# Performance work log

Measured on AMD Instinct MI355X. Metric: run time of the kernel, lower is better.

The kernel has to match this reference:

```python
import jax, jax.numpy as jnp
import numpy as np

MG = (5, 5)          # mesh_grid_size
UP = (17, 17)        # upsample_size
IMG = (512.0, 512.0) # image_size
B = 8192
FC_OUT = MG[0] * MG[1] * 2  # 50
KH = (UP[0] - 1) // (MG[0] - 1) + 1  # 5
KW = (UP[1] - 1) // (MG[1] - 1) + 1  # 5
SH = (UP[0] - 1) // (MG[0] - 1)      # 4
SW = (UP[1] - 1) // (MG[1] - 1)      # 4
L0 = MG[0] - 1
L1 = MG[1] - 1


def _grid(h, w):
    # channel 0: x coords vary along rows (image_size[0]); channel 1: y along cols
    x_t = jnp.broadcast_to(jnp.linspace(0.0, IMG[0], h)[:, None], (h, w))
    y_t = jnp.broadcast_to(jnp.linspace(0.0, IMG[1], w)[None, :], (h, w))
    return jnp.stack([x_t, y_t], 0)  # [2, h, w]


def _unfold22(a):
    # a: [B, 2, H, W] -> [B, (H-1)*(W-1), 4, 2]; 4 = kernel positions row-major, 2 = channel
    p = jnp.stack([a[:, :, :-1, :-1], a[:, :, :-1, 1:],
                   a[:, :, 1:, :-1], a[:, :, 1:, 1:]], axis=2)  # [B,2,4,H-1,W-1]
    return p.reshape(a.shape[0], 2, 4, -1).transpose(0, 3, 2, 1)


def _persp(src, dst):
    # exact 4-point homography solve (torchgeometry.get_perspective_transform)
    x0, y0 = src[..., 0], src[..., 1]
    u, v = dst[..., 0], dst[..., 1]
    z = jnp.zeros_like(x0)
    o = jnp.ones_like(x0)
    ax = jnp.stack([x0, y0, o, z, z, z, -u * x0, -u * y0], -1)  # [N,4,8]
    ay = jnp.stack([z, z, z, x0, y0, o, -v * x0, -v * y0], -1)
    A = jnp.concatenate([ax, ay], 1)                 # [N,8,8]
    bb = jnp.concatenate([u, v], 1)[..., None]       # [N,8,1]
    h = jnp.linalg.solve(A, bb)[..., 0]              # [N,8]
    return jnp.concatenate([h, o[:, :1]], 1).reshape(-1, 3, 3)


def setup_inputs() -> dict:
    key = jax.random.key(0)
    ks = jax.random.split(key, 4)
    def lin(k, i, o):
        return jax.random.normal(k, (i, o), jnp.float32) / jnp.sqrt(i)
    return {
        "x": jax.random.normal(ks[0], (B, 1024), jnp.float32),
        "W1": lin(ks[1], 1024, 1024), "b1": jnp.zeros((1024,), jnp.float32),
        "W2": lin(ks[2], 1024, 2048), "b2": jnp.zeros((2048,), jnp.float32),
        "W3": lin(ks[3], 2048, FC_OUT), "b3": jnp.zeros((FC_OUT,), jnp.float32),
    }


def reference(x, W1, b1, W2, b2, W3, b3):
    Bn = x.shape[0]
    h = jax.nn.relu(x @ W1 + b1)
    h = jax.nn.relu(h @ W2 + b2)
    out = (h @ W3 + b3).reshape(Bn, 2, MG[0], MG[1])  # [B,2,5,5] mesh flow

    # sparse control grid and 2x2 patch corner points
    gs = _grid(MG[0], MG[1])
    src = _unfold22(jnp.broadcast_to(gs[None], (Bn, 2, MG[0], MG[1]))).reshape(-1, 4, 2)
    flow = _unfold22(out).reshape(-1, 4, 2)
    M = _persp(src, src + flow)  # [B*16, 3, 3]

    # dense grid and its unfold2 (kernel KHxKW, stride SHxSW) patch points
    gd = _grid(UP[0], UP[1])  # [2, 17, 17]
    gi = (np.arange(L0) * SH)[:, None, None, None] + np.arange(KH)[None, None, :, None]
    gj = (np.arange(L1) * SW)[None, :, None, None] + np.arange(KW)[None, None, None, :]
    I, J = np.broadcast_arrays(gi, gj)  # [L0,L1,KH,KW]
    pts = gd[:, I, J].transpose(1, 2, 3, 4, 0).reshape(1, L0 * L1, KH * KW, 2)
    pts = jnp.broadcast_to(pts, (Bn, L0 * L1, KH * KW, 2)).reshape(Bn * L0 * L1, KH * KW, 2)

    # transform_points: homogeneous warp + perspective divide
    ph = jnp.concatenate([pts, jnp.ones(pts.shape[:-1] + (1,), pts.dtype)], -1)
    oh = jnp.einsum('nij,npj->npi', M, ph)
    warped = oh[..., :2] / oh[..., 2:3]
    warped = warped.reshape(Bn, L0, L1, KH, KW, 2)

    # Fold: scatter-accumulate overlapping patches
    fold = jnp.zeros((Bn, 2, UP[0], UP[1]), x.dtype)
    for i in range(L0):
        for j in range(L1):
            blk = warped[:, i, j].transpose(0, 3, 1, 2)  # [B,2,KH,KW]
            fold = fold.at[:, :, i * SH:i * SH + KH, j * SW:j * SW + KW].add(blk)

    # boundary rescaling exactly as the torch code: only the 5x5 crossing points
    idx = np.arange(0, UP[0], MG[0] - 1)
    X, Y = np.meshgrid(idx, idx, indexing='xy')
    fold = fold.at[:, :, X, Y].multiply(0.5)
    for (a, b) in ((0, 0), (0, UP[1] - 1), (UP[0] - 1, UP[1] - 1), (UP[0] - 1, 0)):
        fold = fold.at[:, :, a, b].multiply(2.0)

    return fold - gd[None]  # upsampled mesh flow [B,2,17,17]
```

## Files before the change

### kernel.cpp

```cpp
#include <hip/hip_runtime.h>

typedef __bf16 bf16x8 __attribute__((ext_vector_type(8)));
typedef float f32x4 __attribute__((ext_vector_type(4)));

__device__ __forceinline__ unsigned short f2bf(float f) {
  unsigned int u = __builtin_bit_cast(unsigned int, f);
  unsigned int r = (u + 0x7fffu + ((u >> 16) & 1u)) >> 16;
  return (unsigned short)r;
}

__device__ __forceinline__ float bf2f(unsigned short u) {
  unsigned int v = ((unsigned int)u) << 16;
  return __builtin_bit_cast(float, v);
}

__device__ __forceinline__ void load16_lds(const unsigned short* g, unsigned short* l) {
  __builtin_amdgcn_global_load_lds(
      (const __attribute__((address_space(1))) void*)g,
      (__attribute__((address_space(3))) void*)l, 16, 0, 0);
}

__device__ __forceinline__ void wait_vm0() {
  asm volatile("s_waitcnt vmcnt(0)" ::: "memory");
  __builtin_amdgcn_sched_barrier(0);
}
__device__ __forceinline__ void wait_lgkm0() {
  asm volatile("s_waitcnt lgkmcnt(0)" ::: "memory");
  __builtin_amdgcn_sched_barrier(0);
}
__device__ __forceinline__ void barrier_raw() {
  __builtin_amdgcn_sched_barrier(0);
  __builtin_amdgcn_s_barrier();
  __builtin_amdgcn_sched_barrier(0);
}


__global__ __launch_bounds__(256) void prepass(
    const float* __restrict__ x, const float* __restrict__ W1,
    const float* __restrict__ W2, const float* __restrict__ W3,
    unsigned short* __restrict__ xbf, unsigned short* __restrict__ w1t,
    unsigned short* __restrict__ w2t, unsigned short* __restrict__ w3t) {
  __shared__ float tile[32][33];
  const int bid = blockIdx.x;
  const int t = threadIdx.x;
  if (bid < 2048) {
    for (int i = bid * 256 + t; i < 2097152; i += 2048 * 256) {
      float4 f = ((const float4*)x)[i];
      uint2 o;
      o.x = (unsigned)f2bf(f.x) | ((unsigned)f2bf(f.y) << 16);
      o.y = (unsigned)f2bf(f.z) | ((unsigned)f2bf(f.w) << 16);
      ((uint2*)xbf)[i] = o;
    }
  } else if (bid < 3072) {
    int ti = bid - 2048;
    int n0 = (ti & 31) * 32, k0 = (ti >> 5) * 32;
    int tx = t & 31, ty = t >> 5;
    #pragma unroll
    for (int r = 0; r < 32; r += 8)
      tile[ty + r][tx] = W1[(size_t)(k0 + ty + r) * 1024 + n0 + tx];
    __syncthreads();
    #pragma unroll
    for (int r = 0; r < 32; r += 8)
      w1t[(size_t)(n0 + ty + r) * 1024 + k0 + tx] = f2bf(tile[tx][ty + r]);
  } else if (bid < 5120) {
    int ti = bid - 3072;
    int n0 = (ti & 63) * 32, k0 = (ti >> 6) * 32;
    int tx = t & 31, ty = t >> 5;
    #pragma unroll
    for (int r = 0; r < 32; r += 8)
      tile[ty + r][tx] = W2[(size_t)(k0 + ty + r) * 2048 + n0 + tx];
    __syncthreads();
    #pragma unroll
    for (int r = 0; r < 32; r += 8)
      w2t[(size_t)(n0 + ty + r) * 1024 + k0 + tx] = f2bf(tile[tx][ty + r]);
  } else {
    int idx = (bid - 5120) * 256 + t;
    int n = idx >> 11, k = idx & 2047;
    w3t[idx] = f2bf((n < 50) ? W3[(size_t)k * 50 + n] : 0.f);
  }
}


__global__ __launch_bounds__(512, 2) void gemm1_8p(
    const unsigned short* __restrict__ A,
    const unsigned short* __restrict__ Bt,
    const float* __restrict__ bias,
    unsigned short* __restrict__ C) {
  constexpr int K = 1024, N = 1024, NT = 16;
  constexpr int AEL = 256 * 64;
  constexpr int BEL = 128 * 64;
  constexpr int BUF = AEL + BEL;
  __shared__ __align__(16) unsigned short smem[2 * BUF];
  const int t = threadIdx.x;
  const int m0 = blockIdx.x * 256;
  const int n0 = blockIdx.y * 128;
  const int lane = t & 63, wv = t >> 6;
  const int l16 = lane & 15, quad = lane >> 4;
  const int wr = wv >> 1, wc = wv & 1;
  const int rb = wr * 64, cb = wc * 64;

  const int srow = t >> 3;
  const int sg = ((t & 7) ^ (srow & 7)) * 8;
  const unsigned short* Ag0 = A + (size_t)(m0 + srow) * K + sg;
  const unsigned short* Bg0 = Bt + (size_t)(n0 + srow) * K + sg;
  const int ldsO = wv * 8 * 64;

  f32x4 acc[4][4] = {};

  #pragma unroll
  for (int r = 0; r < 4; ++r)
    load16_lds(Ag0 + (size_t)(r * 64) * K, &smem[r * 4096 + ldsO]);
  #pragma unroll
  for (int r = 0; r < 2; ++r)
    load16_lds(Bg0 + (size_t)(r * 64) * K, &smem[AEL + r * 4096 + ldsO]);

  for (int kt = 0; kt < NT; ++kt) {
    unsigned short* Ls = &smem[(kt & 1) * BUF];
    unsigned short* Ln = &smem[((kt + 1) & 1) * BUF];
    const unsigned short* An = Ag0 + (size_t)(kt + 1) * 64;
    const unsigned short* Bn = Bg0 + (size_t)(kt + 1) * 64;
    const bool dost = (kt + 1 < NT);

    wait_vm0();
    barrier_raw();

    bf16x8 af[4], bfr[4];

    #pragma unroll
    for (int ni = 0; ni < 4; ++ni) {
      int row = cb + ni * 16 + l16;
      bfr[ni] = *(const bf16x8*)&Ls[AEL + row * 64 + (quad ^ (row & 7)) * 8];
    }
    #pragma unroll
    for (int mi = 0; mi < 4; ++mi) {
      int row = rb + mi * 16 + l16;
      af[mi] = *(const bf16x8*)&Ls[row * 64 + (quad ^ (row & 7)) * 8];
    }
    if (dost) {
      load16_lds(An, &Ln[ldsO]);
      load16_lds(An + (size_t)64 * K, &Ln[4096 + ldsO]);
      load16_lds(An + (size_t)128 * K, &Ln[8192 + ldsO]);
    }
    barrier_raw();
    wait_lgkm0();
    __builtin_amdgcn_s_setprio(1);
    #pragma unroll
    for (int mi = 0; mi < 4; ++mi)
      #pragma unroll
      for (int ni = 0; ni < 4; ++ni)
        acc[mi][ni] = __builtin_amdgcn_mfma_f32_16x16x32_bf16(
            af[mi], bfr[ni], acc[mi][ni], 0, 0, 0);
    __builtin_amdgcn_s_setprio(0);
    barrier_raw();

    #pragma unroll
    for (int ni = 0; ni < 4; ++ni) {
      int row = cb + ni * 16 + l16;
      bfr[ni] = *(const bf16x8*)&Ls[AEL + row * 64 + ((4 + quad) ^ (row & 7)) * 8];
    }
    #pragma unroll
    for (int mi = 0; mi < 4; ++mi) {
      int row = rb + mi * 16 + l16;
      af[mi] = *(const bf16x8*)&Ls[row * 64 + ((4 + quad) ^ (row & 7)) * 8];
    }
    if (dost) {
      load16_lds(An + (size_t)192 * K, &Ln[12288 + ldsO]);
      load16_lds(Bn, &Ln[AEL + ldsO]);
      load16_lds(Bn + (size_t)64 * K, &Ln[AEL + 4096 + ldsO]);
    }
    barrier_raw();
    wait_lgkm0();
    __builtin_amdgcn_s_setprio(1);
    #pragma unroll
    for (int mi = 0; mi < 4; ++mi)
      #pragma unroll
      for (int ni = 0; ni < 4; ++ni)
        acc[mi][ni] = __builtin_amdgcn_mfma_f32_16x16x32_bf16(
            af[mi], bfr[ni], acc[mi][ni], 0, 0, 0);
    __builtin_amdgcn_s_setprio(0);
    barrier_raw();
  }

  unsigned short* Cs = smem;
  float bv[4];
  #pragma unroll
  for (int ni = 0; ni < 4; ++ni) bv[ni] = bias[n0 + cb + ni * 16 + l16];
  #pragma unroll
  for (int mi = 0; mi < 4; ++mi)
    #pragma unroll
    for (int ni = 0; ni < 4; ++ni)
      #pragma unroll
      for (int r = 0; r < 4; ++r) {
        int row = rb + mi * 16 + quad * 4 + r;
        int col = cb + ni * 16 + l16;
        int pb = (col >> 3) ^ (row & 15);
        Cs[row * 128 + pb * 8 + (col & 7)] = f2bf(fmaxf(acc[mi][ni][r] + bv[ni], 0.f));
      }
  __syncthreads();
  #pragma unroll
  for (int j = 0; j < 8; ++j) {
    int idx = j * 512 + t;
    int row = idx >> 4, cg = idx & 15;
    int pb = cg ^ (row & 15);
    *(uint4*)&C[(size_t)(m0 + row) * N + n0 + cg * 8] =
        *(const uint4*)&Cs[row * 128 + pb * 8];
  }
}


__global__ __launch_bounds__(512, 2) void gemm2_8p(
    const unsigned short* __restrict__ A,
    const unsigned short* __restrict__ Bt,
    const float* __restrict__ bias,
    const unsigned short* __restrict__ W3t,
    unsigned short* __restrict__ part) {
  constexpr int K = 1024, NT = 16;
  constexpr int AEL = 256 * 64;
  constexpr int BUF = 2 * AEL;
  __shared__ __align__(16) unsigned short smem[2 * BUF];
  const int t = threadIdx.x;
  const int m0 = blockIdx.x * 256;
  const int n0 = blockIdx.y * 256;
  const int lane = t & 63, wv = t >> 6;
  const int l16 = lane & 15, quad = lane >> 4;
  const int wr = wv >> 2, wc = wv & 3;
  const int rb = wr * 128, cb = wc * 64;

  const int srow = t >> 3;
  const int sg = ((t & 7) ^ (srow & 7)) * 8;
  const unsigned short* Ag0 = A + (size_t)(m0 + srow) * K + sg;
  const unsigned short* Bg0 = Bt + (size_t)(n0 + srow) * K + sg;
  const int ldsO = wv * 8 * 64;

  f32x4 acc[8][4] = {};

  #pragma unroll
  for (int r = 0; r < 4; ++r) {
    load16_lds(Ag0 + (size_t)(r * 64) * K, &smem[r * 4096 + ldsO]);
    load16_lds(Bg0 + (size_t)(r * 64) * K, &smem[AEL + r * 4096 + ldsO]);
  }

  for (int kt = 0; kt < NT; ++kt) {
    unsigned short* Ls = &smem[(kt & 1) * BUF];
    unsigned short* Ln = &smem[((kt + 1) & 1) * BUF];
    const unsigned short* An = Ag0 + (size_t)(kt + 1) * 64;
    const unsigned short* Bn = Bg0 + (size_t)(kt + 1) * 64;
    const bool dost = (kt + 1 < NT);

    wait_vm0();
    barrier_raw();

    bf16x8 af[4], bfr[4];

    #pragma unroll
    for (int ni = 0; ni < 4; ++ni) {
      int row = cb + ni * 16 + l16;
      bfr[ni] = *(const bf16x8*)&Ls[AEL + row * 64 + (quad ^ (row & 7)) * 8];
    }
    #pragma unroll
    for (int mi = 0; mi < 4; ++mi) {
      int row = rb + mi * 16 + l16;
      af[mi] = *(const bf16x8*)&Ls[row * 64 + (quad ^ (row & 7)) * 8];
    }
    if (dost) {
      load16_lds(An, &Ln[ldsO]);
      load16_lds(An + (size_t)64 * K, &Ln[4096 + ldsO]);
      load16_lds(An + (size_t)128 * K, &Ln[8192 + ldsO]);
    }
    barrier_raw();
    wait_lgkm0();
    __builtin_amdgcn_s_setprio(1);
    #pragma unroll
    for (int mi = 0; mi < 4; ++mi)
      #pragma unroll
      for (int ni = 0; ni < 4; ++ni)
        acc[mi][ni] = __builtin_amdgcn_mfma_f32_16x16x32_bf16(
            af[mi], bfr[ni], acc[mi][ni], 0, 0, 0);
    __builtin_amdgcn_s_setprio(0);
    barrier_raw();

    #pragma unroll
    for (int mi = 0; mi < 4; ++mi) {
      int row = rb + 64 + mi * 16 + l16;
      af[mi] = *(const bf16x8*)&Ls[row * 64 + (quad ^ (row & 7)) * 8];
    }
    if (dost) {
      load16_lds(An + (size_t)192 * K, &Ln[12288 + ldsO]);
      load16_lds(Bn, &Ln[AEL + ldsO]);
      load16_lds(Bn + (size_t)64 * K, &Ln[AEL + 4096 + ldsO]);
    }
    barrier_raw();
    wait_lgkm0();
    __builtin_amdgcn_s_setprio(1);
    #pragma unroll
    for (int mi = 0; mi < 4; ++mi)
      #pragma unroll
      for (int ni = 0; ni < 4; ++ni)
        acc[4 + mi][ni] = __builtin_amdgcn_mfma_f32_16x16x32_bf16(
            af[mi], bfr[ni], acc[4 + mi][ni], 0, 0, 0);
    __builtin_amdgcn_s_setprio(0);
    barrier_raw();

    #pragma unroll
    for (int ni = 0; ni < 4; ++ni) {
      int row = cb + ni * 16 + l16;
      bfr[ni] = *(const bf16x8*)&Ls[AEL + row * 64 + ((4 + quad) ^ (row & 7)) * 8];
    }
    #pragma unroll
    for (int mi = 0; mi < 4; ++mi) {
      int row = rb + 64 + mi * 16 + l16;
      af[mi] = *(const bf16x8*)&Ls[row * 64 + ((4 + quad) ^ (row & 7)) * 8];
    }
    if (dost) {
      load16_lds(Bn + (size_t)128 * K, &Ln[AEL + 8192 + ldsO]);
      load16_lds(Bn + (size_t)192 * K, &Ln[AEL + 12288 + ldsO]);
    }
    barrier_raw();
    wait_lgkm0();
    __builtin_amdgcn_s_setprio(1);
    #pragma unroll
    for (int mi = 0; mi < 4; ++mi)
      #pragma unroll
      for (int ni = 0; ni < 4; ++ni)
        acc[4 + mi][ni] = __builtin_amdgcn_mfma_f32_16x16x32_bf16(
            af[mi], bfr[ni], acc[4 + mi][ni], 0, 0, 0);
    __builtin_amdgcn_s_setprio(0);
    barrier_raw();

    #pragma unroll
    for (int mi = 0; mi < 4; ++mi) {
      int row = rb + mi * 16 + l16;
      af[mi] = *(const bf16x8*)&Ls[row * 64 + ((4 + quad) ^ (row & 7)) * 8];
    }
    barrier_raw();
    wait_lgkm0();
    __builtin_amdgcn_s_setprio(1);
    #pragma unroll
    for (int mi = 0; mi < 4; ++mi)
      #pragma unroll
      for (int ni = 0; ni < 4; ++ni)
        acc[mi][ni] = __builtin_amdgcn_mfma_f32_16x16x32_bf16(
            af[mi], bfr[ni], acc[mi][ni], 0, 0, 0);
    __builtin_amdgcn_s_setprio(0);
    barrier_raw();
  }

  unsigned short* Cs = smem;
  float bv[4];
  #pragma unroll
  for (int ni = 0; ni < 4; ++ni) bv[ni] = bias[n0 + cb + ni * 16 + l16];
  #pragma unroll
  for (int mi = 0; mi < 8; ++mi)
    #pragma unroll
    for (int ni = 0; ni < 4; ++ni)
      #pragma unroll
      for (int r = 0; r < 4; ++r) {
        int row = rb + mi * 16 + quad * 4 + r;
        int col = cb + ni * 16 + l16;
        int pb = (col >> 3) ^ (row & 31);
        Cs[row * 256 + pb * 8 + (col & 7)] = f2bf(fmaxf(acc[mi][ni][r] + bv[ni], 0.f));
      }
  __syncthreads();

  bf16x8 bq[8][4];
  #pragma unroll
  for (int ks = 0; ks < 8; ++ks)
    #pragma unroll
    for (int nt = 0; nt < 4; ++nt)
      bq[ks][nt] = *(const bf16x8*)&W3t[(size_t)(nt * 16 + l16) * 2048 +
                                        n0 + ks * 32 + quad * 8];
  f32x4 acc2[2][4] = {};
  #pragma unroll
  for (int ks = 0; ks < 8; ++ks) {
    bf16x8 af2[2];
    #pragma unroll
    for (int mt = 0; mt < 2; ++mt) {
      int row = wv * 32 + mt * 16 + l16;
      int pb = (ks * 4 + quad) ^ (row & 31);
      af2[mt] = *(const bf16x8*)&Cs[row * 256 + pb * 8];
    }
    #pragma unroll
    for (int mt = 0; mt < 2; ++mt)
      #pragma unroll
      for (int nt = 0; nt < 4; ++nt)
        acc2[mt][nt] = __builtin_amdgcn_mfma_f32_16x16x32_bf16(
            af2[mt], bq[ks][nt], acc2[mt][nt], 0, 0, 0);
  }

  unsigned short* pp = part + (size_t)blockIdx.y * 8192 * 64;
  #pragma unroll
  for (int mt = 0; mt < 2; ++mt)
    #pragma unroll
    for (int nt = 0; nt < 4; ++nt) {
      int col = nt * 16 + l16;
      #pragma unroll
      for (int r = 0; r < 4; ++r) {
        int row = m0 + wv * 32 + mt * 16 + quad * 4 + r;
        pp[(size_t)row * 64 + col] = f2bf(acc2[mt][nt][r]);
      }
    }
}


__global__ __launch_bounds__(256) void geom_reduce(
    const unsigned short* __restrict__ part, const float* __restrict__ b3,
    float* __restrict__ outp) {
  __shared__ float s_out3[16 * 64];
  __shared__ float fold[16 * 578];
  const int t = threadIdx.x;
  const int bbase = blockIdx.x * 16;

  for (int i = t; i < 16 * 578; i += 256) fold[i] = 0.f;
  for (int i = t; i < 1024; i += 256) {
    int m = i >> 6, n = i & 63;
    size_t idx = (size_t)(bbase + m) * 64 + n;
    float v = 0.f;
    #pragma unroll
    for (int z = 0; z < 8; ++z) v += bf2f(part[idx + (size_t)z * 8192 * 64]);
    s_out3[i] = v + ((n < 50) ? b3[n] : 0.f);
  }
  __syncthreads();

  {
    const int bl = t >> 4;
    const int p = t & 15;
    const int pi = p >> 2, pj = p & 3;
    const float* o = &s_out3[bl * 64];

    float u00 = 128.f * pi       + o[pi * 5 + pj];
    float v00 = 128.f * pj       + o[25 + pi * 5 + pj];
    float u01 = 128.f * pi       + o[pi * 5 + pj + 1];
    float v01 = 128.f * (pj + 1) + o[25 + pi * 5 + pj + 1];
    float u10 = 128.f * (pi + 1) + o[(pi + 1) * 5 + pj];
    float v10 = 128.f * pj       + o[25 + (pi + 1) * 5 + pj];
    float u11 = 128.f * (pi + 1) + o[(pi + 1) * 5 + pj + 1];
    float v11 = 128.f * (pj + 1) + o[25 + (pi + 1) * 5 + pj + 1];

    float sx = u00 - u10 + u11 - u01;
    float sy = v00 - v10 + v11 - v01;
    float dx1 = u10 - u11, dx2 = u01 - u11;
    float dy1 = v10 - v11, dy2 = v01 - v11;
    float rden = 1.f / (dx1 * dy2 - dx2 * dy1);
    float g = (sx * dy2 - dx2 * sy) * rden;
    float h = (dx1 * sy - sx * dy1) * rden;
    float a = u10 - u00 + g * u10;
    float b = u01 - u00 + h * u01;
    float c = u00;
    float d = v10 - v00 + g * v10;
    float e = v01 - v00 + h * v01;
    float f = v00;

    #pragma unroll
    for (int ai = 0; ai < 5; ++ai) {
      #pragma unroll
      for (int bi = 0; bi < 5; ++bi) {
        float s = 0.25f * ai, tt = 0.25f * bi;
        float rw = 1.f / (g * s + h * tt + 1.f);
        float xx = (a * s + b * tt + c) * rw;
        float yy = (d * s + e * tt + f) * rw;
        int gi = pi * 4 + ai, gj = pj * 4 + bi;
        atomicAdd(&fold[(bl * 2 + 0) * 289 + gi * 17 + gj], xx);
        atomicAdd(&fold[(bl * 2 + 1) * 289 + gi * 17 + gj], yy);
      }
    }
  }
  __syncthreads();

  for (int i = t; i < 16 * 578; i += 256) {
    int blb = i / 578;
    int rem = i - blb * 578;
    int ch = rem / 289;
    int ij = rem - ch * 289;
    int gi = ij / 17, gj = ij - gi * 17;
    float val = fold[i];
    if ((gi % 4 == 0) && (gj % 4 == 0)) val *= 0.5f;
    if ((gi == 0 || gi == 16) && (gj == 0 || gj == 16)) val *= 2.f;
    val -= (ch == 0) ? 32.f * gi : 32.f * gj;
    outp[(size_t)(bbase + blb) * 578 + rem] = val;
  }
}


extern "C" void kernel_launch(void* const* d_in, const int* in_sizes, int n_in,
                              void* d_out, int out_size, void* d_ws, size_t ws_size,
                              hipStream_t stream) {
  const float* x  = (const float*)d_in[0];
  const float* W1 = (const float*)d_in[1];
  const float* b1 = (const float*)d_in[2];
  const float* W2 = (const float*)d_in[3];
  const float* b2 = (const float*)d_in[4];
  const float* W3 = (const float*)d_in[5];
  const float* b3 = (const float*)d_in[6];
  float* outp = (float*)d_out;

  char* ws = (char*)d_ws;
  unsigned short* xbf = (unsigned short*)ws;
  unsigned short* w1t = (unsigned short*)(ws + (size_t)16 * 1024 * 1024);
  unsigned short* part = (unsigned short*)ws;
  unsigned short* w2t = (unsigned short*)(ws + (size_t)34 * 1024 * 1024);
  unsigned short* w3t = (unsigned short*)(ws + (size_t)38 * 1024 * 1024);
  unsigned short* h1  = (unsigned short*)(ws + (size_t)38 * 1024 * 1024 + 512 * 1024);

  prepass<<<5632, 256, 0, stream>>>(x, W1, W2, W3, xbf, w1t, w2t, w3t);

  gemm1_8p<<<dim3(32, 8), 512, 0, stream>>>(xbf, w1t, b1, h1);
  gemm2_8p<<<dim3(32, 8), 512, 0, stream>>>(h1, w2t, b2, w3t, part);
  geom_reduce<<<512, 256, 0, stream>>>(part, b3, outp);
}
```

Baseline: 201.2 us.

## Split K-tiles into 32-wide halves with four-slot LDS ring and partial vmcnt waits

Both GEMM kernels change from a double-buffered 64-wide K tile with a full vmcnt(0) wait each iteration to a four-slot ring of 32-wide K half-tiles. Loads for half-tiles two steps ahead are issued while the current one is consumed, and waits use vmcnt(3)/vmcnt(4) so in-flight prefetches are not drained. The LDS swizzle becomes a rotation-based layout for 32-element rows. This aims to hide global-to-LDS latency and drop redundant barriers, but the narrower rows may change bank-conflict behaviour and the waitcnt accounting has to match the load counts exactly.

```diff
diff --git a/kernel.cpp b/kernel.cpp
--- a/kernel.cpp
+++ b/kernel.cpp
@@ -22,6 +22,14 @@
 
 __device__ __forceinline__ void wait_vm0() {
   asm volatile("s_waitcnt vmcnt(0)" ::: "memory");
+  __builtin_amdgcn_sched_barrier(0);
+}
+__device__ __forceinline__ void wait_vm3() {
+  asm volatile("s_waitcnt vmcnt(3)" ::: "memory");
+  __builtin_amdgcn_sched_barrier(0);
+}
+__device__ __forceinline__ void wait_vm4() {
+  asm volatile("s_waitcnt vmcnt(4)" ::: "memory");
   __builtin_amdgcn_sched_barrier(0);
 }
 __device__ __forceinline__ void wait_lgkm0() {
@@ -87,60 +95,57 @@
     const float* __restrict__ bias,
     unsigned short* __restrict__ C) {
   constexpr int K = 1024, N = 1024, NT = 16;
-  constexpr int AEL = 256 * 64;
-  constexpr int BEL = 128 * 64;
-  constexpr int BUF = AEL + BEL;
-  __shared__ __align__(16) unsigned short smem[2 * BUF];
+  constexpr int SLOT = 12288;
+  constexpr int BPART = 8192;
+  __shared__ __align__(16) unsigned short smem[4 * SLOT];
   const int t = threadIdx.x;
   const int m0 = blockIdx.x * 256;
   const int n0 = blockIdx.y * 128;
   const int lane = t & 63, wv = t >> 6;
   const int l16 = lane & 15, quad = lane >> 4;
-  const int wr = wv >> 1, wc = wv & 1;
-  const int rb = wr * 64, cb = wc * 64;
-
-  const int srow = t >> 3;
-  const int sg = ((t & 7) ^ (srow & 7)) * 8;
-  const unsigned short* Ag0 = A + (size_t)(m0 + srow) * K + sg;
-  const unsigned short* Bg0 = Bt + (size_t)(n0 + srow) * K + sg;
-  const int ldsO = wv * 8 * 64;
+  const int rb = (wv >> 1) * 64, cb = (wv & 1) * 64;
+
+  const int tr = t >> 2;
+  const int cg = ((t & 3) - (tr >> 1)) & 3;
+  const int ldsS = wv * 512;
+
+  auto stageA = [&](int s, int H) {
+    #pragma unroll
+    for (int i = 0; i < 2; ++i)
+      load16_lds(A + (size_t)(m0 + i * 128 + tr) * K + H * 32 + cg * 8,
+                 &smem[s * SLOT + i * 4096 + ldsS]);
+  };
+  auto stageB = [&](int s, int H) {
+    load16_lds(Bt + (size_t)(n0 + tr) * K + H * 32 + cg * 8,
+               &smem[s * SLOT + BPART + ldsS]);
+  };
+  auto rdA = [&](int s, int row) {
+    return *(const bf16x8*)&smem[s * SLOT + row * 32 +
+                                 ((quad + (row >> 1)) & 3) * 8];
+  };
+  auto rdB = [&](int s, int row) {
+    return *(const bf16x8*)&smem[s * SLOT + BPART + row * 32 +
+                                 ((quad + (row >> 1)) & 3) * 8];
+  };
 
   f32x4 acc[4][4] = {};
 
-  #pragma unroll
-  for (int r = 0; r < 4; ++r)
-    load16_lds(Ag0 + (size_t)(r * 64) * K, &smem[r * 4096 + ldsO]);
-  #pragma unroll
-  for (int r = 0; r < 2; ++r)
-    load16_lds(Bg0 + (size_t)(r * 64) * K, &smem[AEL + r * 4096 + ldsO]);
+  stageA(0, 0); stageB(0, 0);
+  stageA(1, 1); stageB(1, 1);
 
   for (int kt = 0; kt < NT; ++kt) {
-    unsigned short* Ls = &smem[(kt & 1) * BUF];
-    unsigned short* Ln = &smem[((kt + 1) & 1) * BUF];
-    const unsigned short* An = Ag0 + (size_t)(kt + 1) * 64;
-    const unsigned short* Bn = Bg0 + (size_t)(kt + 1) * 64;
+    const int H0 = 2 * kt;
+    const int s0 = H0 & 3, s1 = (H0 + 1) & 3;
     const bool dost = (kt + 1 < NT);
-
-    wait_vm0();
-    barrier_raw();
-
     bf16x8 af[4], bfr[4];
 
-    #pragma unroll
-    for (int ni = 0; ni < 4; ++ni) {
-      int row = cb + ni * 16 + l16;
-      bfr[ni] = *(const bf16x8*)&Ls[AEL + row * 64 + (quad ^ (row & 7)) * 8];
-    }
-    #pragma unroll
-    for (int mi = 0; mi < 4; ++mi) {
-      int row = rb + mi * 16 + l16;
-      af[mi] = *(const bf16x8*)&Ls[row * 64 + (quad ^ (row & 7)) * 8];
-    }
-    if (dost) {
-      load16_lds(An, &Ln[ldsO]);
-      load16_lds(An + (size_t)64 * K, &Ln[4096 + ldsO]);
-      load16_lds(An + (size_t)128 * K, &Ln[8192 + ldsO]);
-    }
+    wait_vm3();
+    barrier_raw();
+    #pragma unroll
+    for (int ni = 0; ni < 4; ++ni) bfr[ni] = rdB(s0, cb + ni * 16 + l16);
+    #pragma unroll
+    for (int mi = 0; mi < 4; ++mi) af[mi] = rdA(s0, rb + mi * 16 + l16);
+    if (dost) { stageA((H0 + 2) & 3, H0 + 2); stageB((H0 + 2) & 3, H0 + 2); }
     barrier_raw();
     wait_lgkm0();
     __builtin_amdgcn_s_setprio(1);
@@ -151,23 +156,14 @@
         acc[mi][ni] = __builtin_amdgcn_mfma_f32_16x16x32_bf16(
             af[mi], bfr[ni], acc[mi][ni], 0, 0, 0);
     __builtin_amdgcn_s_setprio(0);
-    barrier_raw();
-
-    #pragma unroll
-    for (int ni = 0; ni < 4; ++ni) {
-      int row = cb + ni * 16 + l16;
-      bfr[ni] = *(const bf16x8*)&Ls[AEL + row * 64 + ((4 + quad) ^ (row & 7)) * 8];
-    }
-    #pragma unroll
-    for (int mi = 0; mi < 4; ++mi) {
-      int row = rb + mi * 16 + l16;
-      af[mi] = *(const bf16x8*)&Ls[row * 64 + ((4 + quad) ^ (row & 7)) * 8];
-    }
-    if (dost) {
-      load16_lds(An + (size_t)192 * K, &Ln[12288 + ldsO]);
-      load16_lds(Bn, &Ln[AEL + ldsO]);
-      load16_lds(Bn + (size_t)64 * K, &Ln[AEL + 4096 + ldsO]);
-    }
+
+    if (kt == NT - 1) wait_vm0(); else wait_vm3();
+    barrier_raw();
+    #pragma unroll
+    for (int ni = 0; ni < 4; ++ni) bfr[ni] = rdB(s1, cb + ni * 16 + l16);
+    #pragma unroll
+    for (int mi = 0; mi < 4; ++mi) af[mi] = rdA(s1, rb + mi * 16 + l16);
+    if (dost) { stageA((H0 + 3) & 3, H0 + 3); stageB((H0 + 3) & 3, H0 + 3); }
     barrier_raw();
     wait_lgkm0();
     __builtin_amdgcn_s_setprio(1);
@@ -178,8 +174,8 @@
         acc[mi][ni] = __builtin_amdgcn_mfma_f32_16x16x32_bf16(
             af[mi], bfr[ni], acc[mi][ni], 0, 0, 0);
     __builtin_amdgcn_s_setprio(0);
-    barrier_raw();
-  }
+  }
+  barrier_raw();
 
   unsigned short* Cs = smem;
   float bv[4];
@@ -200,9 +196,9 @@
   #pragma unroll
   for (int j = 0; j < 8; ++j) {
     int idx = j * 512 + t;
-    int row = idx >> 4, cg = idx & 15;
-    int pb = cg ^ (row & 15);
-    *(uint4*)&C[(size_t)(m0 + row) * N + n0 + cg * 8] =
+    int row = idx >> 4, cgc = idx & 15;
+    int pb = cgc ^ (row & 15);
+    *(uint4*)&C[(size_t)(m0 + row) * N + n0 + cgc * 8] =
         *(const uint4*)&Cs[row * 128 + pb * 8];
   }
 }
@@ -215,58 +211,60 @@
     const unsigned short* __restrict__ W3t,
     unsigned short* __restrict__ part) {
   constexpr int K = 1024, NT = 16;
-  constexpr int AEL = 256 * 64;
-  constexpr int BUF = 2 * AEL;
-  __shared__ __align__(16) unsigned short smem[2 * BUF];
+  constexpr int SLOT = 16384;
+  constexpr int BPART = 8192;
+  __shared__ __align__(16) unsigned short smem[4 * SLOT];
   const int t = threadIdx.x;
   const int m0 = blockIdx.x * 256;
   const int n0 = blockIdx.y * 256;
   const int lane = t & 63, wv = t >> 6;
   const int l16 = lane & 15, quad = lane >> 4;
-  const int wr = wv >> 2, wc = wv & 3;
-  const int rb = wr * 128, cb = wc * 64;
-
-  const int srow = t >> 3;
-  const int sg = ((t & 7) ^ (srow & 7)) * 8;
-  const unsigned short* Ag0 = A + (size_t)(m0 + srow) * K + sg;
-  const unsigned short* Bg0 = Bt + (size_t)(n0 + srow) * K + sg;
-  const int ldsO = wv * 8 * 64;
+  const int rb = (wv >> 2) * 128, cb = (wv & 3) * 64;
+
+  const int tr = t >> 2;
+  const int cg = ((t & 3) - (tr >> 1)) & 3;
+  const int ldsS = wv * 512;
+
+  auto stageA = [&](int s, int H) {
+    #pragma unroll
+    for (int i = 0; i < 2; ++i)
+      load16_lds(A + (size_t)(m0 + i * 128 + tr) * K + H * 32 + cg * 8,
+                 &smem[s * SLOT + i * 4096 + ldsS]);
+  };
+  auto stageB = [&](int s, int H) {
+    #pragma unroll
+    for (int i = 0; i < 2; ++i)
+      load16_lds(Bt + (size_t)(n0 + i * 128 + tr) * K + H * 32 + cg * 8,
+                 &smem[s * SLOT + BPART + i * 4096 + ldsS]);
+  };
+  auto rdA = [&](int s, int row) {
+    return *(const bf16x8*)&smem[s * SLOT + row * 32 +
+                                 ((quad + (row >> 1)) & 3) * 8];
+  };
+  auto rdB = [&](int s, int row) {
+    return *(const bf16x8*)&smem[s * SLOT + BPART + row * 32 +
+                                 ((quad + (row >> 1)) & 3) * 8];
+  };
 
   f32x4 acc[8][4] = {};
 
-  #pragma unroll
-  for (int r = 0; r < 4; ++r) {
-    load16_lds(Ag0 + (size_t)(r * 64) * K, &smem[r * 4096 + ldsO]);
-    load16_lds(Bg0 + (size_t)(r * 64) * K, &smem[AEL + r * 4096 + ldsO]);
-  }
+  stageA(0, 0); stageB(0, 0);
+  stageA(1, 1); stageB(1, 1);
 
   for (int kt = 0; kt < NT; ++kt) {
-    unsigned short* Ls = &smem[(kt & 1) * BUF];
-    unsigned short* Ln = &smem[((kt + 1) & 1) * BUF];
-    const unsigned short* An = Ag0 + (size_t)(kt + 1) * 64;
-    const unsigned short* Bn = Bg0 + (size_t)(kt + 1) * 64;
+    const int H0 = 2 * kt;
+    const int s0 = H0 & 3, s1 = (H0 + 1) & 3;
+    const int st2 = (H0 + 2) & 3, st3 = (H0 + 3) & 3;
     const bool dost = (kt + 1 < NT);
-
-    wait_vm0();
-    barrier_raw();
-
     bf16x8 af[4], bfr[4];
 
-    #pragma unroll
-    for (int ni = 0; ni < 4; ++ni) {
-      int row = cb + ni * 16 + l16;
-      bfr[ni] = *(const bf16x8*)&Ls[AEL + row * 64 + (quad ^ (row & 7)) * 8];
-    }
-    #pragma unroll
-    for (int mi = 0; mi < 4; ++mi) {
-      int row = rb + mi * 16 + l16;
-      af[mi] = *(const bf16x8*)&Ls[row * 64 + (quad ^ (row & 7)) * 8];
-    }
-    if (dost) {
-      load16_lds(An, &Ln[ldsO]);
-      load16_lds(An + (size_t)64 * K, &Ln[4096 + ldsO]);
-      load16_lds(An + (size_t)128 * K, &Ln[8192 + ldsO]);
-    }
+    wait_vm4();
+    barrier_raw();
+    #pragma unroll
+    for (int ni = 0; ni < 4; ++ni) bfr[ni] = rdB(s0, cb + ni * 16 + l16);
+    #pragma unroll
+    for (int mi = 0; mi < 4; ++mi) af[mi] = rdA(s0, rb + mi * 16 + l16);
+    if (dost) stageA(st2, H0 + 2);
     barrier_raw();
     wait_lgkm0();
     __builtin_amdgcn_s_setprio(1);
@@ -277,18 +275,11 @@
         acc[mi][ni] = __builtin_amdgcn_mfma_f32_16x16x32_bf16(
             af[mi], bfr[ni], acc[mi][ni], 0, 0, 0);
     __builtin_amdgcn_s_setprio(0);
-    barrier_raw();
-
-    #pragma unroll
-    for (int mi = 0; mi < 4; ++mi) {
-      int row = rb + 64 + mi * 16 + l16;
-      af[mi] = *(const bf16x8*)&Ls[row * 64 + (quad ^ (row & 7)) * 8];
-    }
-    if (dost) {
-      load16_lds(An + (size_t)192 * K, &Ln[12288 + ldsO]);
-      load16_lds(Bn, &Ln[AEL + ldsO]);
-      load16_lds(Bn + (size_t)64 * K, &Ln[AEL + 4096 + ldsO]);
-    }
+
+    barrier_raw();
+    #pragma unroll
+    for (int mi = 0; mi < 4; ++mi) af[mi] = rdA(s0, rb + 64 + mi * 16 + l16);
+    if (dost) stageB(st2, H0 + 2);
     barrier_raw();
     wait_lgkm0();
     __builtin_amdgcn_s_setprio(1);
@@ -299,22 +290,14 @@
         acc[4 + mi][ni] = __builtin_amdgcn_mfma_f32_16x16x32_bf16(
             af[mi], bfr[ni], acc[4 + mi][ni], 0, 0, 0);
     __builtin_amdgcn_s_setprio(0);
-    barrier_raw();
-
-    #pragma unroll
-    for (int ni = 0; ni < 4; ++ni) {
-      int row = cb + ni * 16 + l16;
-      bfr[ni] = *(const bf16x8*)&Ls[AEL + row * 64 + ((4 + quad) ^ (row & 7)) * 8];
-    }
-    #pragma unroll
-    for (int mi = 0; mi < 4; ++mi) {
-      int row = rb + 64 + mi * 16 + l16;
-      af[mi] = *(const bf16x8*)&Ls[row * 64 + ((4 + quad) ^ (row & 7)) * 8];
-    }
-    if (dost) {
-      load16_lds(Bn + (size_t)128 * K, &Ln[AEL + 8192 + ldsO]);
-      load16_lds(Bn + (size_t)192 * K, &Ln[AEL + 12288 + ldsO]);
-    }
+
+    if (kt == NT - 1) wait_vm0(); else wait_vm4();
+    barrier_raw();
+    #pragma unroll
+    for (int ni = 0; ni < 4; ++ni) bfr[ni] = rdB(s1, cb + ni * 16 + l16);
+    #pragma unroll
+    for (int mi = 0; mi < 4; ++mi) af[mi] = rdA(s1, rb + 64 + mi * 16 + l16);
+    if (dost) stageA(st3, H0 + 3);
     barrier_raw();
     wait_lgkm0();
     __builtin_amdgcn_s_setprio(1);
@@ -325,13 +308,11 @@
         acc[4 + mi][ni] = __builtin_amdgcn_mfma_f32_16x16x32_bf16(
             af[mi], bfr[ni], acc[4 + mi][ni], 0, 0, 0);
     __builtin_amdgcn_s_setprio(0);
-    barrier_raw();
-
-    #pragma unroll
-    for (int mi = 0; mi < 4; ++mi) {
-      int row = rb + mi * 16 + l16;
-      af[mi] = *(const bf16x8*)&Ls[row * 64 + ((4 + quad) ^ (row & 7)) * 8];
-    }
+
+    barrier_raw();
+    #pragma unroll
+    for (int mi = 0; mi < 4; ++mi) af[mi] = rdA(s1, rb + mi * 16 + l16);
+    if (dost) stageB(st3, H0 + 3);
     barrier_raw();
     wait_lgkm0();
     __builtin_amdgcn_s_setprio(1);
@@ -342,8 +323,8 @@
         acc[mi][ni] = __builtin_amdgcn_mfma_f32_16x16x32_bf16(
             af[mi], bfr[ni], acc[mi][ni], 0, 0, 0);
     __builtin_amdgcn_s_setprio(0);
-    barrier_raw();
-  }
+  }
+  barrier_raw();
 
   unsigned short* Cs = smem;
   float bv[4];
```

Measured after the change: 200.1 us. No clear change (-0.6%).
